# Kernel optimization log

Measured on AMD Instinct MI355X. Metric: run time of the kernel, lower is better.

The kernel has to match this reference:

```python
import jax, jax.numpy as jnp
import numpy as np

N, E, F, H = 100000, 1000000, 128, 64
BN_EPS = 1e-3  # keras BatchNormalization default epsilon


def setup_inputs() -> dict:
    key = jax.random.key(0)
    k_x, k_src, k_dst, k_w = jax.random.split(key, 4)
    node_features = jax.random.normal(k_x, (N, F), dtype=jnp.float32)
    # Ensure every node appears at least once as a source so that
    # deg**-0.5 is finite (the original code implicitly assumes this).
    src = jnp.concatenate([
        jnp.arange(N, dtype=jnp.int32),
        jax.random.randint(k_src, (E - N,), 0, N, dtype=jnp.int32),
    ])
    dst = jax.random.randint(k_dst, (E,), 0, N, dtype=jnp.int32)
    edge_index = jnp.stack([src, dst], axis=1)  # [E, 2]
    # glorot_uniform for kernel
    limit = np.sqrt(6.0 / (F + H)).astype(np.float32)
    W = jax.random.uniform(k_w, (F, H), dtype=jnp.float32, minval=-limit, maxval=limit)
    b = jnp.zeros((H,), dtype=jnp.float32)
    bn_gamma = jnp.ones((H,), dtype=jnp.float32)
    bn_beta = jnp.zeros((H,), dtype=jnp.float32)
    bn_mean = jnp.zeros((H,), dtype=jnp.float32)
    bn_var = jnp.ones((H,), dtype=jnp.float32)
    return dict(node_features=node_features, W=W, b=b, bn_gamma=bn_gamma,
                bn_beta=bn_beta, bn_mean=bn_mean, bn_var=bn_var,
                edge_index=edge_index)


def reference(node_features, W, b, bn_gamma, bn_beta, bn_mean, bn_var, edge_index):
    n = node_features.shape[0]
    src = edge_index[:, 0]
    dst = edge_index[:, 1]
    # Dense transform; dropout is identity in inference (training=False).
    h = node_features @ W + b  # [N, H]
    # Out-degree per node (segments keyed by src, matching the TF code).
    deg = jax.ops.segment_sum(jnp.ones(src.shape, h.dtype), src, num_segments=n)  # [N]
    inv_sqrt_deg = deg ** -0.5
    # Per-edge symmetric-style scaling: deg(src)^-0.5 * deg(dst)^-0.5 * h[dst]
    edge_scale = inv_sqrt_deg[src] * inv_sqrt_deg[dst]  # [E]
    neigh = edge_scale[:, None] * h[dst]  # [E, H]
    agg = 0.5 * jax.ops.segment_sum(neigh, src, num_segments=n)  # [N, H]
    # Self term: segment_mean of deg(src) * h[src] over src segments.
    self_term = deg[src][:, None] * h[src]  # [E, H]
    self_sum = jax.ops.segment_sum(self_term, src, num_segments=n)  # [N, H]
    self_mean = self_sum / jnp.maximum(deg, 1.0)[:, None]
    agg = agg + 0.5 * self_mean
    # BatchNormalization in inference mode.
    out = (agg - bn_mean) * (bn_gamma * jax.lax.rsqrt(bn_var + BN_EPS)) + bn_beta
    return out
```

## Files before the change

kernel.cpp:

```cpp
#include <hip/hip_runtime.h>

#define BN_EPS 0.001f
#define CAP 48

__device__ __forceinline__ float bf2f(unsigned short u) {
  return __uint_as_float(((unsigned)u) << 16);
}
__device__ __forceinline__ unsigned short f2bf(float f) {
  unsigned u = __float_as_uint(f);
  u += 0x7fffu + ((u >> 16) & 1u);
  return (unsigned short)(u >> 16);
}

__global__ __launch_bounds__(256) void k_fused(
    const float* __restrict__ X, const float* __restrict__ W,
    const float* __restrict__ B,
    unsigned short* __restrict__ hb, int N, int Gg,
    const int2* __restrict__ ei, int* __restrict__ cnt,
    int* __restrict__ ell, int E, int Gs) {
  __shared__ float Ws[128 * 64];
  __shared__ unsigned short Xs[64 * 132];

  int g = blockIdx.x / 7;
  int r = blockIdx.x % 7;

  if (r >= 2) {
    int chunk = g * 5 + (r - 2);
    if (chunk >= Gs) return;
    int e = chunk * 256 + threadIdx.x;
    if (e < E) {
      int2 sd = ei[e];
      int pos = atomicAdd(&cnt[sd.x], 1);
      if (pos < CAP) ell[(size_t)sd.x * CAP + pos] = sd.y;
    }
    return;
  }

  int tile = g * 2 + r;
  if (tile >= Gg) return;
  int tid = threadIdx.x;

  const float4* W4 = (const float4*)W;
  for (int i = tid; i < 2048; i += 256) *(float4*)&Ws[i * 4] = W4[i];

  int row0 = tile * 64;
  const float4* X4 = (const float4*)(X + (size_t)row0 * 128);
  int avail = (N - row0) * 128;
  for (int i = tid * 4; i < 8192; i += 1024) {
    int rr = i >> 7, c = i & 127;
    float4 v = (i + 3 < avail) ? X4[i >> 2] : make_float4(0.f, 0.f, 0.f, 0.f);
    ushort4 bv;
    bv.x = f2bf(v.x); bv.y = f2bf(v.y); bv.z = f2bf(v.z); bv.w = f2bf(v.w);
    *(ushort4*)&Xs[rr * 132 + c] = bv;
  }
  __syncthreads();

  int tx = tid & 15, ty = tid >> 4;
  int c4 = tx * 4;
  int rbase = ty * 4;
  float4 bb = *(const float4*)&B[c4];
  float4 acc[4];
  acc[0] = bb; acc[1] = bb; acc[2] = bb; acc[3] = bb;

  #pragma unroll 4
  for (int k = 0; k < 128; k += 4) {
    float4 w0 = *(const float4*)&Ws[(k + 0) * 64 + c4];
    float4 w1 = *(const float4*)&Ws[(k + 1) * 64 + c4];
    float4 w2 = *(const float4*)&Ws[(k + 2) * 64 + c4];
    float4 w3 = *(const float4*)&Ws[(k + 3) * 64 + c4];
    #pragma unroll
    for (int rr = 0; rr < 4; ++rr) {
      ushort4 xu = *(const ushort4*)&Xs[(rbase + rr) * 132 + k];
      float xvx = bf2f(xu.x), xvy = bf2f(xu.y), xvz = bf2f(xu.z), xvw = bf2f(xu.w);
      acc[rr].x = fmaf(xvx, w0.x, acc[rr].x); acc[rr].y = fmaf(xvx, w0.y, acc[rr].y);
      acc[rr].z = fmaf(xvx, w0.z, acc[rr].z); acc[rr].w = fmaf(xvx, w0.w, acc[rr].w);
      acc[rr].x = fmaf(xvy, w1.x, acc[rr].x); acc[rr].y = fmaf(xvy, w1.y, acc[rr].y);
      acc[rr].z = fmaf(xvy, w1.z, acc[rr].z); acc[rr].w = fmaf(xvy, w1.w, acc[rr].w);
      acc[rr].x = fmaf(xvz, w2.x, acc[rr].x); acc[rr].y = fmaf(xvz, w2.y, acc[rr].y);
      acc[rr].z = fmaf(xvz, w2.z, acc[rr].z); acc[rr].w = fmaf(xvz, w2.w, acc[rr].w);
      acc[rr].x = fmaf(xvw, w3.x, acc[rr].x); acc[rr].y = fmaf(xvw, w3.y, acc[rr].y);
      acc[rr].z = fmaf(xvw, w3.z, acc[rr].z); acc[rr].w = fmaf(xvw, w3.w, acc[rr].w);
    }
  }

  #pragma unroll
  for (int rr = 0; rr < 4; ++rr) {
    int row = row0 + rbase + rr;
    if (row < N) {
      ushort4 hv;
      hv.x = f2bf(acc[rr].x); hv.y = f2bf(acc[rr].y);
      hv.z = f2bf(acc[rr].z); hv.w = f2bf(acc[rr].w);
      *(ushort4*)&hb[(size_t)row * 64 + c4] = hv;
    }
  }
}

__global__ __launch_bounds__(256) void k_aggfinal(const int* __restrict__ cnt,
                                                  const int* __restrict__ ell,
                                                  const unsigned int* __restrict__ hb32,
                                                  const float* __restrict__ gamma,
                                                  const float* __restrict__ beta,
                                                  const float* __restrict__ mean,
                                                  const float* __restrict__ var,
                                                  float* __restrict__ out, int N) {
  int wave = threadIdx.x >> 6;
  int lane = threadIdx.x & 63;
  int sub  = lane >> 5;
  int fp   = lane & 31;
  int node = blockIdx.x * 8 + wave * 2 + sub;
  if (node >= N) return;

  int c0 = cnt[node];
  int c = (c0 < CAP) ? c0 : CAP;
  const int* row = &ell[(size_t)node * CAP];

  float ax = 0.f, ay = 0.f;
  int p = 0;
  for (; p + 4 <= c; p += 4) {
    int d0 = row[p], d1 = row[p + 1], d2 = row[p + 2], d3 = row[p + 3];
    float s0 = rsqrtf((float)cnt[d0]);
    float s1 = rsqrtf((float)cnt[d1]);
    float s2 = rsqrtf((float)cnt[d2]);
    float s3 = rsqrtf((float)cnt[d3]);
    unsigned u0 = hb32[(size_t)d0 * 32 + fp];
    unsigned u1 = hb32[(size_t)d1 * 32 + fp];
    unsigned u2 = hb32[(size_t)d2 * 32 + fp];
    unsigned u3 = hb32[(size_t)d3 * 32 + fp];
    ax = fmaf(s0, __uint_as_float(u0 << 16), ax);
    ay = fmaf(s0, __uint_as_float(u0 & 0xffff0000u), ay);
    ax = fmaf(s1, __uint_as_float(u1 << 16), ax);
    ay = fmaf(s1, __uint_as_float(u1 & 0xffff0000u), ay);
    ax = fmaf(s2, __uint_as_float(u2 << 16), ax);
    ay = fmaf(s2, __uint_as_float(u2 & 0xffff0000u), ay);
    ax = fmaf(s3, __uint_as_float(u3 << 16), ax);
    ay = fmaf(s3, __uint_as_float(u3 & 0xffff0000u), ay);
  }
  for (; p < c; ++p) {
    int d = row[p];
    float s = rsqrtf((float)cnt[d]);
    unsigned u = hb32[(size_t)d * 32 + fp];
    ax = fmaf(s, __uint_as_float(u << 16), ax);
    ay = fmaf(s, __uint_as_float(u & 0xffff0000u), ay);
  }

  int j = fp * 2;
  unsigned us = hb32[(size_t)node * 32 + fp];
  float hx = __uint_as_float(us << 16);
  float hy = __uint_as_float(us & 0xffff0000u);

  float degf = (float)c0;
  float isd_n = rsqrtf((float)((c0 > 0) ? c0 : 1));
  float rx = 0.5f * (isd_n * ax + degf * hx);
  float ry = 0.5f * (isd_n * ay + degf * hy);

  float2 gm = *(const float2*)&gamma[j];
  float2 bt = *(const float2*)&beta[j];
  float2 mn = *(const float2*)&mean[j];
  float2 vr = *(const float2*)&var[j];
  float2 o;
  o.x = (rx - mn.x) * (gm.x * rsqrtf(vr.x + BN_EPS)) + bt.x;
  o.y = (ry - mn.y) * (gm.y * rsqrtf(vr.y + BN_EPS)) + bt.y;
  *(float2*)&out[(size_t)node * 64 + j] = o;
}

extern "C" void kernel_launch(void* const* d_in, const int* in_sizes, int n_in,
                              void* d_out, int out_size, void* d_ws, size_t ws_size,
                              hipStream_t stream) {
  const float* X     = (const float*)d_in[0];
  const float* W     = (const float*)d_in[1];
  const float* B     = (const float*)d_in[2];
  const float* gamma = (const float*)d_in[3];
  const float* beta  = (const float*)d_in[4];
  const float* mean  = (const float*)d_in[5];
  const float* var   = (const float*)d_in[6];
  const int2*  ei    = (const int2*)d_in[7];

  int N = in_sizes[0] / 128;
  int E = in_sizes[7] / 2;

  unsigned short* hb  = (unsigned short*)d_ws;
  int*            ell = (int*)(hb + (size_t)N * 64);
  int*            cnt = ell + (size_t)N * CAP;
  float*          out = (float*)d_out;

  hipMemsetAsync(cnt, 0, (size_t)N * sizeof(int), stream);

  int Gg = (N + 63) / 64;
  int Gs = (E + 255) / 256;
  int g7 = (Gg + 1) / 2;
  int g5 = (Gs + 4) / 5;
  int groups = (g7 > g5) ? g7 : g5;
  k_fused<<<groups * 7, 256, 0, stream>>>(X, W, B, hb, N, Gg, ei, cnt, ell, E, Gs);

  k_aggfinal<<<(N + 7) / 8, 256, 0, stream>>>(cnt, ell, (const unsigned int*)hb,
                                              gamma, beta, mean, var, out, N);
}
```

Measured before the change: 202.4 us.

## Use bf16 MFMA for dense transform and unroll gather loop by eight

Replaces the scalar FMA tile GEMM with MFMA 16x16x32 bf16 instructions. W is converted to bf16 and stored transposed with an XOR swizzle in shared memory, and each lane loads its X fragment straight from global memory, so the X staging buffer goes away. Separately, the aggregation loop now processes eight neighbours per iteration, giving more gathers in flight. The GEMM is a small part of a kernel dominated by the edge scatter and gather, so any gain is bounded, and the X loads are now less coalesced per lane.

```diff
diff --git a/kernel.cpp b/kernel.cpp
--- a/kernel.cpp
+++ b/kernel.cpp
@@ -2,6 +2,9 @@
 
 #define BN_EPS 0.001f
 #define CAP 48
+
+typedef __attribute__((ext_vector_type(8))) short bf16x8;
+typedef __attribute__((ext_vector_type(4))) float f32x4;
 
 __device__ __forceinline__ float bf2f(unsigned short u) {
   return __uint_as_float(((unsigned)u) << 16);
@@ -18,8 +21,7 @@
     unsigned short* __restrict__ hb, int N, int Gg,
     const int2* __restrict__ ei, int* __restrict__ cnt,
     int* __restrict__ ell, int E, int Gs) {
-  __shared__ float Ws[128 * 64];
-  __shared__ unsigned short Xs[64 * 132];
+  __shared__ float WtF[4096];
 
   int g = blockIdx.x / 7;
   int r = blockIdx.x % 7;
@@ -38,59 +40,60 @@
 
   int tile = g * 2 + r;
   if (tile >= Gg) return;
+
+  char* Wt = (char*)WtF;
   int tid = threadIdx.x;
-
-  const float4* W4 = (const float4*)W;
-  for (int i = tid; i < 2048; i += 256) *(float4*)&Ws[i * 4] = W4[i];
+  for (int i = tid; i < 8192; i += 256) {
+    int k = i >> 6, col = i & 63;
+    unsigned short v = f2bf(W[i]);
+    *(unsigned short*)(Wt + ((col << 8) | ((k << 1) ^ ((col & 7) << 4)))) = v;
+  }
+  __syncthreads();
+
+  int lane = tid & 63;
+  int w = tid >> 6;
+  int l15 = lane & 15;
+  int lk = lane >> 4;
 
   int row0 = tile * 64;
-  const float4* X4 = (const float4*)(X + (size_t)row0 * 128);
-  int avail = (N - row0) * 128;
-  for (int i = tid * 4; i < 8192; i += 1024) {
-    int rr = i >> 7, c = i & 127;
-    float4 v = (i + 3 < avail) ? X4[i >> 2] : make_float4(0.f, 0.f, 0.f, 0.f);
-    ushort4 bv;
-    bv.x = f2bf(v.x); bv.y = f2bf(v.y); bv.z = f2bf(v.z); bv.w = f2bf(v.w);
-    *(ushort4*)&Xs[rr * 132 + c] = bv;
-  }
-  __syncthreads();
-
-  int tx = tid & 15, ty = tid >> 4;
-  int c4 = tx * 4;
-  int rbase = ty * 4;
-  float4 bb = *(const float4*)&B[c4];
-  float4 acc[4];
-  acc[0] = bb; acc[1] = bb; acc[2] = bb; acc[3] = bb;
-
-  #pragma unroll 4
-  for (int k = 0; k < 128; k += 4) {
-    float4 w0 = *(const float4*)&Ws[(k + 0) * 64 + c4];
-    float4 w1 = *(const float4*)&Ws[(k + 1) * 64 + c4];
-    float4 w2 = *(const float4*)&Ws[(k + 2) * 64 + c4];
-    float4 w3 = *(const float4*)&Ws[(k + 3) * 64 + c4];
-    #pragma unroll
-    for (int rr = 0; rr < 4; ++rr) {
-      ushort4 xu = *(const ushort4*)&Xs[(rbase + rr) * 132 + k];
-      float xvx = bf2f(xu.x), xvy = bf2f(xu.y), xvz = bf2f(xu.z), xvw = bf2f(xu.w);
-      acc[rr].x = fmaf(xvx, w0.x, acc[rr].x); acc[rr].y = fmaf(xvx, w0.y, acc[rr].y);
-      acc[rr].z = fmaf(xvx, w0.z, acc[rr].z); acc[rr].w = fmaf(xvx, w0.w, acc[rr].w);
-      acc[rr].x = fmaf(xvy, w1.x, acc[rr].x); acc[rr].y = fmaf(xvy, w1.y, acc[rr].y);
-      acc[rr].z = fmaf(xvy, w1.z, acc[rr].z); acc[rr].w = fmaf(xvy, w1.w, acc[rr].w);
-      acc[rr].x = fmaf(xvz, w2.x, acc[rr].x); acc[rr].y = fmaf(xvz, w2.y, acc[rr].y);
-      acc[rr].z = fmaf(xvz, w2.z, acc[rr].z); acc[rr].w = fmaf(xvz, w2.w, acc[rr].w);
-      acc[rr].x = fmaf(xvw, w3.x, acc[rr].x); acc[rr].y = fmaf(xvw, w3.y, acc[rr].y);
-      acc[rr].z = fmaf(xvw, w3.z, acc[rr].z); acc[rr].w = fmaf(xvw, w3.w, acc[rr].w);
-    }
-  }
-
+  int rA = row0 + w * 16 + l15;
+  bool rowok = rA < N;
+  const float* xp = X + (size_t)rA * 128 + (lk << 3);
+
+  f32x4 acc[4];
   #pragma unroll
-  for (int rr = 0; rr < 4; ++rr) {
-    int row = row0 + rbase + rr;
-    if (row < N) {
-      ushort4 hv;
-      hv.x = f2bf(acc[rr].x); hv.y = f2bf(acc[rr].y);
-      hv.z = f2bf(acc[rr].z); hv.w = f2bf(acc[rr].w);
-      *(ushort4*)&hb[(size_t)row * 64 + c4] = hv;
+  for (int n = 0; n < 4; ++n) {
+    float bv = B[(n << 4) + l15];
+    acc[n] = (f32x4){bv, bv, bv, bv};
+  }
+
+  #pragma unroll
+  for (int kb = 0; kb < 4; ++kb) {
+    bf16x8 af = {0, 0, 0, 0, 0, 0, 0, 0};
+    if (rowok) {
+      float4 x0 = *(const float4*)(xp + kb * 32);
+      float4 x1 = *(const float4*)(xp + kb * 32 + 4);
+      af[0] = (short)f2bf(x0.x); af[1] = (short)f2bf(x0.y);
+      af[2] = (short)f2bf(x0.z); af[3] = (short)f2bf(x0.w);
+      af[4] = (short)f2bf(x1.x); af[5] = (short)f2bf(x1.y);
+      af[6] = (short)f2bf(x1.z); af[7] = (short)f2bf(x1.w);
+    }
+    int kbyte = (kb << 6) | (lk << 4);
+    #pragma unroll
+    for (int n = 0; n < 4; ++n) {
+      int col = (n << 4) + l15;
+      bf16x8 bfr = *(const bf16x8*)(Wt + ((col << 8) | (kbyte ^ ((col & 7) << 4))));
+      acc[n] = __builtin_amdgcn_mfma_f32_16x16x32_bf16(af, bfr, acc[n], 0, 0, 0);
+    }
+  }
+
+  int rbase = row0 + w * 16 + (lk << 2);
+  #pragma unroll
+  for (int n = 0; n < 4; ++n) {
+    #pragma unroll
+    for (int q = 0; q < 4; ++q) {
+      int row = rbase + q;
+      if (row < N) hb[(size_t)row * 64 + (n << 4) + l15] = f2bf(acc[n][q]);
     }
   }
 }
@@ -116,7 +119,23 @@
 
   float ax = 0.f, ay = 0.f;
   int p = 0;
-  for (; p + 4 <= c; p += 4) {
+  for (; p + 8 <= c; p += 8) {
+    int d[8];
+    #pragma unroll
+    for (int q = 0; q < 8; ++q) d[q] = row[p + q];
+    float s[8];
+    #pragma unroll
+    for (int q = 0; q < 8; ++q) s[q] = rsqrtf((float)cnt[d[q]]);
+    unsigned u[8];
+    #pragma unroll
+    for (int q = 0; q < 8; ++q) u[q] = hb32[(size_t)d[q] * 32 + fp];
+    #pragma unroll
+    for (int q = 0; q < 8; ++q) {
+      ax = fmaf(s[q], __uint_as_float(u[q] << 16), ax);
+      ay = fmaf(s[q], __uint_as_float(u[q] & 0xffff0000u), ay);
+    }
+  }
+  if (p + 4 <= c) {
     int d0 = row[p], d1 = row[p + 1], d2 = row[p + 2], d3 = row[p + 3];
     float s0 = rsqrtf((float)cnt[d0]);
     float s1 = rsqrtf((float)cnt[d1]);
@@ -134,6 +153,7 @@
     ay = fmaf(s2, __uint_as_float(u2 & 0xffff0000u), ay);
     ax = fmaf(s3, __uint_as_float(u3 << 16), ax);
     ay = fmaf(s3, __uint_as_float(u3 & 0xffff0000u), ay);
+    p += 4;
   }
   for (; p < c; ++p) {
     int d = row[p];
```

After: 209.3 us. +3.4%, slower.
